# Kernel optimization log

Hardware: AMD Instinct MI355X
Metric: run time of the kernel (lower is better)

The kernel has to match this reference:

```python
import jax, jax.numpy as jnp
import numpy as np

N, E, H, T = 50000, 100000, 512, 6  # nodes, edges, hidden_size, num_edge_types


def setup_inputs() -> dict:
    key = jax.random.key(0)
    ks = jax.random.split(key, 14)
    xav = 1.0 / np.sqrt(H)
    return {
        "statement_embeddings": jax.random.normal(ks[0], (N, H), jnp.float32),
        "source_indices": jax.random.randint(ks[1], (E,), 0, N, dtype=jnp.int32),
        "dest_indices": jax.random.randint(ks[2], (E,), 0, N, dtype=jnp.int32),
        "edge_types": jax.random.randint(ks[3], (E,), 0, T, dtype=jnp.int32),
        "num_nodes": N,
        "hidden_size": H,
        # edge_dense: Dense(features=6*H), xavier_uniform kernel, tiny-normal bias
        "W_edge": jax.random.uniform(ks[4], (H, T * H), jnp.float32, -1.0, 1.0) * np.sqrt(6.0 / (H + T * H)),
        "b_edge": jax.random.normal(ks[5], (T * H,), jnp.float32) * 1e-6,
        # GRUCell params (flax convention: input denses have bias; hidden r/z denses no bias; hidden n dense has bias)
        "W_ir": jax.random.normal(ks[6], (H, H), jnp.float32) * xav,
        "W_iz": jax.random.normal(ks[7], (H, H), jnp.float32) * xav,
        "W_in": jax.random.normal(ks[8], (H, H), jnp.float32) * xav,
        "b_ir": jnp.zeros((H,), jnp.float32),
        "b_iz": jnp.zeros((H,), jnp.float32),
        "b_in": jnp.zeros((H,), jnp.float32),
        "W_hr": jax.random.normal(ks[9], (H, H), jnp.float32) * xav,
        "W_hz": jax.random.normal(ks[10], (H, H), jnp.float32) * xav,
        "W_hn": jax.random.normal(ks[11], (H, H), jnp.float32) * xav,
        "b_hn": jnp.zeros((H,), jnp.float32),
    }


def reference(statement_embeddings, source_indices, dest_indices, edge_types,
              num_nodes, hidden_size,
              W_edge, b_edge,
              W_ir, W_iz, W_in, b_ir, b_iz, b_in,
              W_hr, W_hz, W_hn, b_hn):
    num_edge_types = 6
    # gather source node embeddings: [E, H]
    src = statement_embeddings[source_indices]
    # per-edge dense to all edge types: [E, T*H] -> [E, T, H]
    all_types = (src @ W_edge + b_edge).reshape(-1, num_edge_types, hidden_size)
    # select the slice for each edge's type: [E, H]
    msgs = jnp.take_along_axis(all_types, edge_types[:, None, None], axis=1)[:, 0, :]
    # scatter-add to destination nodes: [N, H]
    proposed = jax.ops.segment_sum(msgs, dest_indices, num_segments=num_nodes)
    # GRU update: inputs=proposed, carry=statement_embeddings
    h = statement_embeddings
    r = jax.nn.sigmoid(proposed @ W_ir + b_ir + h @ W_hr)
    z = jax.nn.sigmoid(proposed @ W_iz + b_iz + h @ W_hz)
    n = jnp.tanh(proposed @ W_in + b_in + r * (h @ W_hn + b_hn))
    return (1.0 - z) * n + z * h
```

## Files before the change

### kernel.cpp

```cpp
#include <hip/hip_runtime.h>
#include <hip/hip_bf16.h>
#include <math.h>

#define H 512
#define NT 6

#define EBM 128
#define EBN 128
#define EBK 32
#define GBM 128
#define GBN 64
#define GBK 32

typedef short bf16x8 __attribute__((ext_vector_type(8)));
typedef float f32x4 __attribute__((ext_vector_type(4)));

__device__ __forceinline__ float sigmoidf_(float x) { return 1.0f / (1.0f + expf(-x)); }

__device__ __forceinline__ unsigned short f2bf(float f) {
    unsigned int u = __float_as_uint(f);
    u = (u + 0x7FFF + ((u >> 16) & 1)) >> 16;
    return (unsigned short)u;
}

__device__ __forceinline__ void glds16(const void* g, void* l) {
    __builtin_amdgcn_global_load_lds((const __attribute__((address_space(1))) unsigned int*)g,
                                     (__attribute__((address_space(3))) unsigned int*)l,
                                     16, 0, 0);
}

__global__ void hist_kernel(const int* __restrict__ etype, int E, int* __restrict__ meta) {
    __shared__ int lh[NT];
    if (threadIdx.x < NT) lh[threadIdx.x] = 0;
    __syncthreads();
    int i = blockIdx.x * blockDim.x + threadIdx.x;
    if (i < E) atomicAdd(&lh[etype[i]], 1);
    __syncthreads();
    if (threadIdx.x < NT) {
        int c = lh[threadIdx.x];
        if (c) atomicAdd(&meta[threadIdx.x], c);
    }
}

__global__ void prefix_kernel(int* __restrict__ meta) {
    if (threadIdx.x == 0 && blockIdx.x == 0) {
        int acc = 0;
        for (int t = 0; t < NT; ++t) {
            meta[8 + t]  = acc;
            meta[16 + t] = acc;
            acc += ((meta[t] + EBM - 1) / EBM) * EBM;
        }
        meta[8 + NT] = acc;
    }
}

__global__ void scatter_perm_kernel(const int* __restrict__ etype, int E,
                                    int* __restrict__ meta, int* __restrict__ perm) {
    __shared__ int lcount[NT];
    __shared__ int lbase[NT];
    const int tid = threadIdx.x;
    if (tid < NT) lcount[tid] = 0;
    __syncthreads();
    int i = blockIdx.x * blockDim.x + tid;
    int t = 0, rank = 0;
    if (i < E) {
        t = etype[i];
        rank = atomicAdd(&lcount[t], 1);
    }
    __syncthreads();
    if (tid < NT) {
        int c = lcount[tid];
        lbase[tid] = c ? atomicAdd(&meta[16 + tid], c) : 0;
    }
    __syncthreads();
    if (i < E) perm[lbase[t] + rank] = i;
}

__global__ void conv_bf16_kernel(const float* __restrict__ in, unsigned short* __restrict__ out, int n4) {
    int i = blockIdx.x * blockDim.x + threadIdx.x;
    if (i < n4) {
        float4 v = ((const float4*)in)[i];
        ushort4 o;
        o.x = f2bf(v.x); o.y = f2bf(v.y); o.z = f2bf(v.z); o.w = f2bf(v.w);
        ((ushort4*)out)[i] = o;
    }
}

__global__ void conv_gru_w_kernel(const float* __restrict__ Wir, const float* __restrict__ Wiz,
                                  const float* __restrict__ Win, const float* __restrict__ Whr,
                                  const float* __restrict__ Whz, const float* __restrict__ Whn,
                                  unsigned short* __restrict__ Brt, unsigned short* __restrict__ Bzt,
                                  unsigned short* __restrict__ Bnit, unsigned short* __restrict__ Bnht) {
    int idx = blockIdx.x * blockDim.x + threadIdx.x;
    if (idx >= 512 * 1024) return;
    int n = idx >> 10;
    int k = idx & 1023;
    int kk = k & 511;
    const float* wr = (k < 512) ? Wir : Whr;
    const float* wz = (k < 512) ? Wiz : Whz;
    Brt[idx] = f2bf(wr[kk * H + n]);
    Bzt[idx] = f2bf(wz[kk * H + n]);
    if (k < 512) Bnit[n * H + k]  = f2bf(Win[k * H + n]);
    else         Bnht[n * H + kk] = f2bf(Whn[kk * H + n]);
}

__global__ void conv_edge_w_kernel(const float* __restrict__ W_edge, unsigned short* __restrict__ WeT) {
    int idx = blockIdx.x * blockDim.x + threadIdx.x;
    if (idx >= 3072 * 512) return;
    int n = idx >> 9;
    int k = idx & 511;
    WeT[idx] = f2bf(W_edge[(size_t)k * (NT * H) + n]);
}

__global__ __launch_bounds__(256)
void edge_msg_mfma(const unsigned short* __restrict__ emb_bf,
                   const int* __restrict__ src_idx,
                   const int* __restrict__ dst_idx,
                   const float* __restrict__ b_edge,
                   const unsigned short* __restrict__ WeT,
                   const int* __restrict__ meta,
                   const int* __restrict__ perm,
                   float* __restrict__ proposed)
{
    __shared__ short As[2][EBM * EBK];
    __shared__ short Bs[2][EBN * EBK];
    __shared__ int ls_src[EBM];
    __shared__ int ls_dst[EBM];

    const int rowBase = blockIdx.y * EBM;
    if (rowBase >= meta[8 + NT]) return;
    int t = 0;
    while (rowBase >= meta[8 + t + 1]) ++t;

    const int colBase = blockIdx.x * EBN;
    const int tid = threadIdx.x;

    if (tid < EBM) {
        int e = perm[rowBase + tid];
        int s = 0, d = -1;
        if (e >= 0) { s = src_idx[e] * H; d = dst_idx[e] * H; }
        ls_src[tid] = s;
        ls_dst[tid] = d;
    }
    __syncthreads();

    const int lane = tid & 63;
    const int wave = tid >> 6;
    const int wm = (wave >> 1) * 64;
    const int wn = (wave & 1) * 64;
    const int q = lane >> 4;
    const int r = lane & 15;

    const int rA   = tid >> 2;
    const int slot = (tid & 3) * 8;

    const int s0 = ls_src[rA];
    const int s1 = ls_src[64 + rA];
    const size_t b0 = ((size_t)(t * H + colBase + rA)) * H + slot;
    const size_t b1 = ((size_t)(t * H + colBase + 64 + rA)) * H + slot;

    f32x4 acc[4][4];
    #pragma unroll
    for (int i = 0; i < 4; ++i)
        #pragma unroll
        for (int j = 0; j < 4; ++j) acc[i][j] = (f32x4){0.f, 0.f, 0.f, 0.f};

#define ESTAGE(K0, B)                                                   \
    {                                                                   \
        glds16(emb_bf + (size_t)s0 + (K0) + slot, &As[B][tid * 8]);     \
        glds16(emb_bf + (size_t)s1 + (K0) + slot, &As[B][(256 + tid) * 8]); \
        glds16(WeT + b0 + (K0), &Bs[B][tid * 8]);                       \
        glds16(WeT + b1 + (K0), &Bs[B][(256 + tid) * 8]);               \
    }

    ESTAGE(0, 0);
    __syncthreads();
    int cur = 0;

    for (int k0 = 0; k0 < H; k0 += EBK) {
        if (k0 + EBK < H) ESTAGE(k0 + EBK, cur ^ 1);

        bf16x8 a[4];
        #pragma unroll
        for (int i = 0; i < 4; ++i)
            a[i] = *(const bf16x8*)&As[cur][(wm + i * 16 + r) * EBK + q * 8];
        #pragma unroll
        for (int j = 0; j < 4; ++j) {
            bf16x8 b = *(const bf16x8*)&Bs[cur][(wn + j * 16 + r) * EBK + q * 8];
            #pragma unroll
            for (int i = 0; i < 4; ++i)
                acc[i][j] = __builtin_amdgcn_mfma_f32_16x16x32_bf16(a[i], b, acc[i][j], 0, 0, 0);
        }
        __syncthreads();
        cur ^= 1;
    }
#undef ESTAGE

    int cols[4];
    float bias[4];
    #pragma unroll
    for (int j = 0; j < 4; ++j) {
        cols[j] = colBase + wn + j * 16 + r;
        bias[j] = b_edge[t * H + cols[j]];
    }
    #pragma unroll
    for (int i = 0; i < 4; ++i) {
        #pragma unroll
        for (int reg = 0; reg < 4; ++reg) {
            int row = wm + i * 16 + q * 4 + reg;
            int d = ls_dst[row];
            if (d < 0) continue;
            #pragma unroll
            for (int j = 0; j < 4; ++j)
                atomicAdd(&proposed[(size_t)d + cols[j]], acc[i][j][reg] + bias[j]);
        }
    }
}

__global__ __launch_bounds__(256)
void gru_mfma(const unsigned short* __restrict__ prop_bf,
              const unsigned short* __restrict__ emb_bf,
              const float* __restrict__ emb_f32,
              const unsigned short* __restrict__ Brt,
              const unsigned short* __restrict__ Bzt,
              const unsigned short* __restrict__ Bnit,
              const unsigned short* __restrict__ Bnht,
              const float* __restrict__ bir, const float* __restrict__ biz,
              const float* __restrict__ bin, const float* __restrict__ bhn,
              float* __restrict__ out, int N)
{
    __shared__ short As[2][GBM * GBK];
    __shared__ short Brs[2][GBN * GBK];
    __shared__ short Bzs[2][GBN * GBK];
    __shared__ short Bns[2][GBN * GBK];

    int wg = blockIdx.y * gridDim.x + blockIdx.x;
    const int nwg = gridDim.x * gridDim.y;
    if ((nwg & 7) == 0) {
        const int cpx = nwg >> 3;
        wg = (wg & 7) * cpx + (wg >> 3);
    }
    const int rowBase = (wg / gridDim.x) * GBM;
    const int colBase = (wg % gridDim.x) * GBN;

    const int tid = threadIdx.x;
    const int lane = tid & 63;
    const int wave = tid >> 6;
    const int wm = (wave >> 1) * 64;
    const int wn = (wave & 1) * 32;
    const int q = lane >> 4;
    const int r = lane & 15;

    const int rA   = tid >> 2;
    const int slot = (tid & 3) * 8;

    const size_t aOff0  = (size_t)(rowBase + rA) * H + slot;
    const size_t aOff1  = (size_t)(rowBase + 64 + rA) * H + slot;
    const size_t bOffRZ = (size_t)(colBase + rA) * 1024 + slot;
    const size_t bOffN  = (size_t)(colBase + rA) * 512 + slot;

    f32x4 accR[4][2], accZ[4][2], accNI[4][2], accNH[4][2];
    #pragma unroll
    for (int i = 0; i < 4; ++i)
        #pragma unroll
        for (int j = 0; j < 2; ++j) {
            accR[i][j] = (f32x4){0.f, 0.f, 0.f, 0.f};
            accZ[i][j] = accR[i][j];
            accNI[i][j] = accR[i][j];
            accNH[i][j] = accR[i][j];
        }

#define GSTAGE(S, B)                                                     \
    {                                                                    \
        const unsigned short* Asrc_ = ((S) < 16) ? prop_bf : emb_bf;     \
        const unsigned short* Bn_   = ((S) < 16) ? Bnit : Bnht;          \
        const int kk_ = ((S) & 15) * GBK;                                \
        const int k0_ = (S) * GBK;                                       \
        glds16(Asrc_ + aOff0 + kk_, &As[B][tid * 8]);                    \
        glds16(Asrc_ + aOff1 + kk_, &As[B][(256 + tid) * 8]);            \
        glds16(Brt + bOffRZ + k0_, &Brs[B][tid * 8]);                    \
        glds16(Bzt + bOffRZ + k0_, &Bzs[B][tid * 8]);                    \
        glds16(Bn_ + bOffN + kk_, &Bns[B][tid * 8]);                     \
    }

#define GCOMPUTE(ACCN, B)                                                                            \
    {                                                                                                \
        bf16x8 a[4];                                                                                 \
        _Pragma("unroll")                                                                            \
        for (int i = 0; i < 4; ++i)                                                                  \
            a[i] = *(const bf16x8*)&As[B][(wm + i * 16 + r) * GBK + q * 8];                          \
        _Pragma("unroll")                                                                            \
        for (int j = 0; j < 2; ++j) {                                                                \
            bf16x8 br = *(const bf16x8*)&Brs[B][(wn + j * 16 + r) * GBK + q * 8];                    \
            bf16x8 bz = *(const bf16x8*)&Bzs[B][(wn + j * 16 + r) * GBK + q * 8];                    \
            bf16x8 bn = *(const bf16x8*)&Bns[B][(wn + j * 16 + r) * GBK + q * 8];                    \
            _Pragma("unroll")                                                                        \
            for (int i = 0; i < 4; ++i) {                                                            \
                accR[i][j] = __builtin_amdgcn_mfma_f32_16x16x32_bf16(a[i], br, accR[i][j], 0, 0, 0); \
                accZ[i][j] = __builtin_amdgcn_mfma_f32_16x16x32_bf16(a[i], bz, accZ[i][j], 0, 0, 0); \
                ACCN[i][j] = __builtin_amdgcn_mfma_f32_16x16x32_bf16(a[i], bn, ACCN[i][j], 0, 0, 0); \
            }                                                                                        \
        }                                                                                            \
    }

    GSTAGE(0, 0);
    __syncthreads();
    int cur = 0;

    for (int s = 0; s < 16; ++s) {
        GSTAGE(s + 1, cur ^ 1);
        GCOMPUTE(accNI, cur);
        __syncthreads();
        cur ^= 1;
    }
    for (int s = 16; s < 32; ++s) {
        if (s < 31) GSTAGE(s + 1, cur ^ 1);
        GCOMPUTE(accNH, cur);
        __syncthreads();
        cur ^= 1;
    }
#undef GSTAGE
#undef GCOMPUTE

    #pragma unroll
    for (int j = 0; j < 2; ++j) {
        const int col = colBase + wn + j * 16 + r;
        const float vbir = bir[col], vbiz = biz[col], vbin = bin[col], vbhn = bhn[col];
        #pragma unroll
        for (int i = 0; i < 4; ++i) {
            #pragma unroll
            for (int reg = 0; reg < 4; ++reg) {
                const int row = rowBase + wm + i * 16 + q * 4 + reg;
                if (row >= N) continue;
                float rg = sigmoidf_(accR[i][j][reg] + vbir);
                float zg = sigmoidf_(accZ[i][j][reg] + vbiz);
                float ng = tanhf(accNI[i][j][reg] + vbin + rg * (accNH[i][j][reg] + vbhn));
                float h = emb_f32[(size_t)row * H + col];
                out[(size_t)row * H + col] = (1.0f - zg) * ng + zg * h;
            }
        }
    }
}

extern "C" void kernel_launch(void* const* d_in, const int* in_sizes, int n_in,
                              void* d_out, int out_size, void* d_ws, size_t ws_size,
                              hipStream_t stream) {
    const float* emb     = (const float*)d_in[0];
    const int*   src_idx = (const int*)d_in[1];
    const int*   dst_idx = (const int*)d_in[2];
    const int*   etype   = (const int*)d_in[3];
    const float* W_edge  = (const float*)d_in[6];
    const float* b_edge  = (const float*)d_in[7];
    const float* Wir = (const float*)d_in[8];
    const float* Wiz = (const float*)d_in[9];
    const float* Win = (const float*)d_in[10];
    const float* bir = (const float*)d_in[11];
    const float* biz = (const float*)d_in[12];
    const float* bin = (const float*)d_in[13];
    const float* Whr = (const float*)d_in[14];
    const float* Whz = (const float*)d_in[15];
    const float* Whn = (const float*)d_in[16];
    const float* bhn = (const float*)d_in[17];

    const int E = in_sizes[1];
    const int N = in_sizes[0] / H;
    const int NH = N * H;

    char* ws = (char*)d_ws;
    float*          proposed = (float*)ws;                       ws += (size_t)NH * 4;
    unsigned short* prop_bf  = (unsigned short*)ws;              ws += (size_t)NH * 2;
    unsigned short* emb_bf   = (unsigned short*)ws;              ws += (size_t)NH * 2;
    unsigned short* Brt      = (unsigned short*)ws;              ws += 512 * 1024 * 2;
    unsigned short* Bzt      = (unsigned short*)ws;              ws += 512 * 1024 * 2;
    unsigned short* Bnit     = (unsigned short*)ws;              ws += 512 * 512 * 2;
    unsigned short* Bnht     = (unsigned short*)ws;              ws += 512 * 512 * 2;
    unsigned short* WeT      = (unsigned short*)ws;              ws += 3072 * 512 * 2;
    int*            meta     = (int*)ws;                         ws += 32 * 4;
    int*            perm     = (int*)ws;
    const int maxRowTiles = (E + EBM - 1) / EBM + NT;

    hipMemsetAsync(proposed, 0, (size_t)NH * 4, stream);
    hipMemsetAsync(meta, 0, 32 * 4, stream);
    hipMemsetAsync(perm, 0xFF, (size_t)maxRowTiles * EBM * 4, stream);

    const int n4 = NH / 4;
    conv_bf16_kernel<<<(n4 + 255) / 256, 256, 0, stream>>>(emb, emb_bf, n4);
    conv_gru_w_kernel<<<(512 * 1024 + 255) / 256, 256, 0, stream>>>(
        Wir, Wiz, Win, Whr, Whz, Whn, Brt, Bzt, Bnit, Bnht);
    conv_edge_w_kernel<<<(3072 * 512 + 255) / 256, 256, 0, stream>>>(W_edge, WeT);

    hist_kernel<<<(E + 255) / 256, 256, 0, stream>>>(etype, E, meta);
    prefix_kernel<<<1, 64, 0, stream>>>(meta);
    scatter_perm_kernel<<<(E + 255) / 256, 256, 0, stream>>>(etype, E, meta, perm);

    dim3 egrid(H / EBN, maxRowTiles);
    edge_msg_mfma<<<egrid, 256, 0, stream>>>(emb_bf, src_idx, dst_idx, b_edge, WeT,
                                             meta, perm, proposed);

    conv_bf16_kernel<<<(n4 + 255) / 256, 256, 0, stream>>>(proposed, prop_bf, n4);

    dim3 ggrid(H / GBN, (N + GBM - 1) / GBM);
    gru_mfma<<<ggrid, 256, 0, stream>>>(prop_bf, emb_bf, emb, Brt, Bzt, Bnit, Bnht,
                                        bir, biz, bin, bhn, (float*)d_out, N);
}
```

Before: 877.7 us.

## Deepen LDS pipelining to four buffers with vmcnt-based waits and single barrier

Both the edge-message GEMM and the GRU GEMM move from double-buffered LDS staging to a four-slot ring that prefetches two stages ahead. Each iteration now waits only until the current stage's async global-to-LDS loads have landed (s_waitcnt vmcnt with an outstanding-load count) and uses one barrier, instead of a full __syncthreads at the end of every step. The aim is to keep more loads in flight and hide global memory latency behind MFMA work. In exchange LDS use doubles, which may lower occupancy. Correctness depends on the hard-coded vmcnt values matching the number of loads issued per stage, and on the four-slot ring leaving enough distance that a slot is not overwritten while a slower wave is still reading it.

```diff
diff --git a/kernel.cpp b/kernel.cpp
--- a/kernel.cpp
+++ b/kernel.cpp
@@ -28,6 +28,13 @@
                                      (__attribute__((address_space(3))) unsigned int*)l,
                                      16, 0, 0);
 }
+
+#define WAITBAR(N)                                         \
+    {                                                      \
+        asm volatile("s_waitcnt vmcnt(" #N ")" ::: "memory"); \
+        __builtin_amdgcn_s_barrier();                      \
+        asm volatile("" ::: "memory");                     \
+    }
 
 __global__ void hist_kernel(const int* __restrict__ etype, int E, int* __restrict__ meta) {
     __shared__ int lh[NT];
@@ -122,8 +129,8 @@
                    const int* __restrict__ perm,
                    float* __restrict__ proposed)
 {
-    __shared__ short As[2][EBM * EBK];
-    __shared__ short Bs[2][EBN * EBK];
+    __shared__ short As[4][EBM * EBK];
+    __shared__ short Bs[4][EBN * EBK];
     __shared__ int ls_src[EBM];
     __shared__ int ls_dst[EBM];
 
@@ -165,36 +172,43 @@
         #pragma unroll
         for (int j = 0; j < 4; ++j) acc[i][j] = (f32x4){0.f, 0.f, 0.f, 0.f};
 
-#define ESTAGE(K0, B)                                                   \
-    {                                                                   \
-        glds16(emb_bf + (size_t)s0 + (K0) + slot, &As[B][tid * 8]);     \
-        glds16(emb_bf + (size_t)s1 + (K0) + slot, &As[B][(256 + tid) * 8]); \
-        glds16(WeT + b0 + (K0), &Bs[B][tid * 8]);                       \
-        glds16(WeT + b1 + (K0), &Bs[B][(256 + tid) * 8]);               \
+#define ESTAGE(S, B)                                                        \
+    {                                                                       \
+        const int k0_ = (S) * EBK;                                          \
+        glds16(emb_bf + (size_t)s0 + k0_ + slot, &As[B][tid * 8]);          \
+        glds16(emb_bf + (size_t)s1 + k0_ + slot, &As[B][(256 + tid) * 8]);  \
+        glds16(WeT + b0 + k0_, &Bs[B][tid * 8]);                            \
+        glds16(WeT + b1 + k0_, &Bs[B][(256 + tid) * 8]);                    \
+    }
+
+#define ECOMPUTE(B)                                                                          \
+    {                                                                                        \
+        bf16x8 a[4];                                                                         \
+        _Pragma("unroll")                                                                    \
+        for (int i = 0; i < 4; ++i)                                                          \
+            a[i] = *(const bf16x8*)&As[B][(wm + i * 16 + r) * EBK + q * 8];                  \
+        _Pragma("unroll")                                                                    \
+        for (int j = 0; j < 4; ++j) {                                                        \
+            bf16x8 b = *(const bf16x8*)&Bs[B][(wn + j * 16 + r) * EBK + q * 8];              \
+            _Pragma("unroll")                                                                \
+            for (int i = 0; i < 4; ++i)                                                      \
+                acc[i][j] = __builtin_amdgcn_mfma_f32_16x16x32_bf16(a[i], b, acc[i][j], 0, 0, 0); \
+        }                                                                                    \
     }
 
     ESTAGE(0, 0);
-    __syncthreads();
-    int cur = 0;
-
-    for (int k0 = 0; k0 < H; k0 += EBK) {
-        if (k0 + EBK < H) ESTAGE(k0 + EBK, cur ^ 1);
-
-        bf16x8 a[4];
-        #pragma unroll
-        for (int i = 0; i < 4; ++i)
-            a[i] = *(const bf16x8*)&As[cur][(wm + i * 16 + r) * EBK + q * 8];
-        #pragma unroll
-        for (int j = 0; j < 4; ++j) {
-            bf16x8 b = *(const bf16x8*)&Bs[cur][(wn + j * 16 + r) * EBK + q * 8];
-            #pragma unroll
-            for (int i = 0; i < 4; ++i)
-                acc[i][j] = __builtin_amdgcn_mfma_f32_16x16x32_bf16(a[i], b, acc[i][j], 0, 0, 0);
-        }
-        __syncthreads();
-        cur ^= 1;
-    }
+    ESTAGE(1, 1);
+    for (int s = 0; s < 14; ++s) {
+        ESTAGE(s + 2, (s + 2) & 3);
+        WAITBAR(8);
+        ECOMPUTE(s & 3);
+    }
+    WAITBAR(4);
+    ECOMPUTE(2);
+    WAITBAR(0);
+    ECOMPUTE(3);
 #undef ESTAGE
+#undef ECOMPUTE
 
     int cols[4];
     float bias[4];
@@ -229,10 +243,10 @@
               const float* __restrict__ bin, const float* __restrict__ bhn,
               float* __restrict__ out, int N)
 {
-    __shared__ short As[2][GBM * GBK];
-    __shared__ short Brs[2][GBN * GBK];
-    __shared__ short Bzs[2][GBN * GBK];
-    __shared__ short Bns[2][GBN * GBK];
+    __shared__ short As[4][GBM * GBK];
+    __shared__ short Brs[4][GBN * GBK];
+    __shared__ short Bzs[4][GBN * GBK];
+    __shared__ short Bns[4][GBN * GBK];
 
     int wg = blockIdx.y * gridDim.x + blockIdx.x;
     const int nwg = gridDim.x * gridDim.y;
@@ -304,21 +318,21 @@
     }
 
     GSTAGE(0, 0);
-    __syncthreads();
-    int cur = 0;
-
+    GSTAGE(1, 1);
     for (int s = 0; s < 16; ++s) {
-        GSTAGE(s + 1, cur ^ 1);
-        GCOMPUTE(accNI, cur);
-        __syncthreads();
-        cur ^= 1;
-    }
-    for (int s = 16; s < 32; ++s) {
-        if (s < 31) GSTAGE(s + 1, cur ^ 1);
-        GCOMPUTE(accNH, cur);
-        __syncthreads();
-        cur ^= 1;
-    }
+        GSTAGE(s + 2, (s + 2) & 3);
+        WAITBAR(10);
+        GCOMPUTE(accNI, s & 3);
+    }
+    for (int s = 16; s < 30; ++s) {
+        GSTAGE(s + 2, (s + 2) & 3);
+        WAITBAR(10);
+        GCOMPUTE(accNH, s & 3);
+    }
+    WAITBAR(5);
+    GCOMPUTE(accNH, 2);
+    WAITBAR(0);
+    GCOMPUTE(accNH, 3);
 #undef GSTAGE
 #undef GCOMPUTE
 
```

After: 994.8 us. 1.13x slower.

## Triple-buffer GEMM pipelines, interleave activations, use fixed-point int atomics

Applied to the files above, without the earlier changes.

Both MFMA GEMMs move from a double-buffered loop with a full barrier each step to a fully unrolled three-stage LDS pipeline. Each step waits with s_waitcnt vmcnt(N) plus a raw barrier, so global-to-LDS loads stay in flight during compute. Proposed and embedding activations are stored interleaved in one row-concatenated bf16 buffer [prop|emb] with a unified transposed N-gate weight, which simplifies GRU staging. The scatter-add now uses integer atomics on values scaled by 65536, trading float atomics for fixed-point rounding and possible overflow on large sums. The GRU kernel also gains a launch-bounds occupancy hint of 2.

```diff
diff --git a/kernel.cpp b/kernel.cpp
--- a/kernel.cpp
+++ b/kernel.cpp
@@ -12,6 +12,9 @@
 #define GBN 64
 #define GBK 32
 
+#define PSCALE 65536.0f
+#define PINV   (1.0f / 65536.0f)
+
 typedef short bf16x8 __attribute__((ext_vector_type(8)));
 typedef float f32x4 __attribute__((ext_vector_type(4)));
 
@@ -28,6 +31,13 @@
                                      (__attribute__((address_space(3))) unsigned int*)l,
                                      16, 0, 0);
 }
+
+#define WAITBAR(N)                                                        \
+    {                                                                     \
+        asm volatile("s_waitcnt vmcnt(" #N ") lgkmcnt(0)" ::: "memory");  \
+        __builtin_amdgcn_s_barrier();                                     \
+        asm volatile("" ::: "memory");                                    \
+    }
 
 __global__ void hist_kernel(const int* __restrict__ etype, int E, int* __restrict__ meta) {
     __shared__ int lh[NT];
@@ -76,13 +86,29 @@
     if (i < E) perm[lbase[t] + rank] = i;
 }
 
-__global__ void conv_bf16_kernel(const float* __restrict__ in, unsigned short* __restrict__ out, int n4) {
+__global__ void conv_to_ah(const float* __restrict__ in, unsigned short* __restrict__ AH,
+                           int n4, int half) {
     int i = blockIdx.x * blockDim.x + threadIdx.x;
     if (i < n4) {
         float4 v = ((const float4*)in)[i];
         ushort4 o;
         o.x = f2bf(v.x); o.y = f2bf(v.y); o.z = f2bf(v.z); o.w = f2bf(v.w);
-        ((ushort4*)out)[i] = o;
+        int row = i >> 7;
+        int c4  = i & 127;
+        ((ushort4*)AH)[row * 256 + half * 128 + c4] = o;
+    }
+}
+
+__global__ void conv_i2ah(const int* __restrict__ in, unsigned short* __restrict__ AH, int n4) {
+    int i = blockIdx.x * blockDim.x + threadIdx.x;
+    if (i < n4) {
+        int4 v = ((const int4*)in)[i];
+        ushort4 o;
+        o.x = f2bf((float)v.x * PINV); o.y = f2bf((float)v.y * PINV);
+        o.z = f2bf((float)v.z * PINV); o.w = f2bf((float)v.w * PINV);
+        int row = i >> 7;
+        int c4  = i & 127;
+        ((ushort4*)AH)[row * 256 + c4] = o;
     }
 }
 
@@ -90,7 +116,7 @@
                                   const float* __restrict__ Win, const float* __restrict__ Whr,
                                   const float* __restrict__ Whz, const float* __restrict__ Whn,
                                   unsigned short* __restrict__ Brt, unsigned short* __restrict__ Bzt,
-                                  unsigned short* __restrict__ Bnit, unsigned short* __restrict__ Bnht) {
+                                  unsigned short* __restrict__ Bnt) {
     int idx = blockIdx.x * blockDim.x + threadIdx.x;
     if (idx >= 512 * 1024) return;
     int n = idx >> 10;
@@ -98,10 +124,10 @@
     int kk = k & 511;
     const float* wr = (k < 512) ? Wir : Whr;
     const float* wz = (k < 512) ? Wiz : Whz;
+    const float* wn = (k < 512) ? Win : Whn;
     Brt[idx] = f2bf(wr[kk * H + n]);
     Bzt[idx] = f2bf(wz[kk * H + n]);
-    if (k < 512) Bnit[n * H + k]  = f2bf(Win[k * H + n]);
-    else         Bnht[n * H + kk] = f2bf(Whn[kk * H + n]);
+    Bnt[idx] = f2bf(wn[kk * H + n]);
 }
 
 __global__ void conv_edge_w_kernel(const float* __restrict__ W_edge, unsigned short* __restrict__ WeT) {
@@ -113,17 +139,17 @@
 }
 
 __global__ __launch_bounds__(256)
-void edge_msg_mfma(const unsigned short* __restrict__ emb_bf,
+void edge_msg_mfma(const unsigned short* __restrict__ AH,
                    const int* __restrict__ src_idx,
                    const int* __restrict__ dst_idx,
                    const float* __restrict__ b_edge,
                    const unsigned short* __restrict__ WeT,
                    const int* __restrict__ meta,
                    const int* __restrict__ perm,
-                   float* __restrict__ proposed)
+                   int* __restrict__ proposed)
 {
-    __shared__ short As[2][EBM * EBK];
-    __shared__ short Bs[2][EBN * EBK];
+    __shared__ short As[3][EBM * EBK];
+    __shared__ short Bs[3][EBN * EBK];
     __shared__ int ls_src[EBM];
     __shared__ int ls_dst[EBM];
 
@@ -137,8 +163,8 @@
 
     if (tid < EBM) {
         int e = perm[rowBase + tid];
-        int s = 0, d = -1;
-        if (e >= 0) { s = src_idx[e] * H; d = dst_idx[e] * H; }
+        int s = 512, d = -1;
+        if (e >= 0) { s = src_idx[e] * 1024 + 512; d = dst_idx[e] * H; }
         ls_src[tid] = s;
         ls_dst[tid] = d;
     }
@@ -165,36 +191,45 @@
         #pragma unroll
         for (int j = 0; j < 4; ++j) acc[i][j] = (f32x4){0.f, 0.f, 0.f, 0.f};
 
-#define ESTAGE(K0, B)                                                   \
-    {                                                                   \
-        glds16(emb_bf + (size_t)s0 + (K0) + slot, &As[B][tid * 8]);     \
-        glds16(emb_bf + (size_t)s1 + (K0) + slot, &As[B][(256 + tid) * 8]); \
-        glds16(WeT + b0 + (K0), &Bs[B][tid * 8]);                       \
-        glds16(WeT + b1 + (K0), &Bs[B][(256 + tid) * 8]);               \
+#define ESTAGE(S, B)                                                         \
+    {                                                                        \
+        glds16(AH + (size_t)s0 + (S) * EBK + slot, &As[B][tid * 8]);         \
+        glds16(AH + (size_t)s1 + (S) * EBK + slot, &As[B][(256 + tid) * 8]); \
+        glds16(WeT + b0 + (S) * EBK, &Bs[B][tid * 8]);                       \
+        glds16(WeT + b1 + (S) * EBK, &Bs[B][(256 + tid) * 8]);               \
+    }
+
+#define ECOMPUTE(B)                                                                               \
+    {                                                                                             \
+        bf16x8 a[4];                                                                              \
+        _Pragma("unroll")                                                                         \
+        for (int i = 0; i < 4; ++i)                                                               \
+            a[i] = *(const bf16x8*)&As[B][(wm + i * 16 + r) * EBK + q * 8];                       \
+        _Pragma("unroll")                                                                         \
+        for (int j = 0; j < 4; ++j) {                                                             \
+            bf16x8 b = *(const bf16x8*)&Bs[B][(wn + j * 16 + r) * EBK + q * 8];                   \
+            _Pragma("unroll")                                                                     \
+            for (int i = 0; i < 4; ++i)                                                           \
+                acc[i][j] = __builtin_amdgcn_mfma_f32_16x16x32_bf16(a[i], b, acc[i][j], 0, 0, 0); \
+        }                                                                                         \
+    }
+
+#define ESTEP(S)                         \
+    {                                    \
+        WAITBAR(4);                      \
+        ESTAGE((S) + 2, ((S) + 2) % 3);  \
+        ECOMPUTE((S) % 3);               \
     }
 
     ESTAGE(0, 0);
-    __syncthreads();
-    int cur = 0;
-
-    for (int k0 = 0; k0 < H; k0 += EBK) {
-        if (k0 + EBK < H) ESTAGE(k0 + EBK, cur ^ 1);
-
-        bf16x8 a[4];
-        #pragma unroll
-        for (int i = 0; i < 4; ++i)
-            a[i] = *(const bf16x8*)&As[cur][(wm + i * 16 + r) * EBK + q * 8];
-        #pragma unroll
-        for (int j = 0; j < 4; ++j) {
-            bf16x8 b = *(const bf16x8*)&Bs[cur][(wn + j * 16 + r) * EBK + q * 8];
-            #pragma unroll
-            for (int i = 0; i < 4; ++i)
-                acc[i][j] = __builtin_amdgcn_mfma_f32_16x16x32_bf16(a[i], b, acc[i][j], 0, 0, 0);
-        }
-        __syncthreads();
-        cur ^= 1;
-    }
+    ESTAGE(1, 1);
+    ESTEP(0)  ESTEP(1)  ESTEP(2)  ESTEP(3)  ESTEP(4)  ESTEP(5)  ESTEP(6)
+    ESTEP(7)  ESTEP(8)  ESTEP(9)  ESTEP(10) ESTEP(11) ESTEP(12) ESTEP(13)
+    { WAITBAR(4); ECOMPUTE(2); }
+    { WAITBAR(0); ECOMPUTE(0); }
 #undef ESTAGE
+#undef ECOMPUTE
+#undef ESTEP
 
     int cols[4];
     float bias[4];
@@ -212,27 +247,26 @@
             if (d < 0) continue;
             #pragma unroll
             for (int j = 0; j < 4; ++j)
-                atomicAdd(&proposed[(size_t)d + cols[j]], acc[i][j][reg] + bias[j]);
+                atomicAdd(&proposed[(size_t)d + cols[j]],
+                          __float2int_rn((acc[i][j][reg] + bias[j]) * PSCALE));
         }
     }
 }
 
-__global__ __launch_bounds__(256)
-void gru_mfma(const unsigned short* __restrict__ prop_bf,
-              const unsigned short* __restrict__ emb_bf,
+__global__ __launch_bounds__(256, 2)
+void gru_mfma(const unsigned short* __restrict__ AH,
               const float* __restrict__ emb_f32,
               const unsigned short* __restrict__ Brt,
               const unsigned short* __restrict__ Bzt,
-              const unsigned short* __restrict__ Bnit,
-              const unsigned short* __restrict__ Bnht,
+              const unsigned short* __restrict__ Bnt,
               const float* __restrict__ bir, const float* __restrict__ biz,
               const float* __restrict__ bin, const float* __restrict__ bhn,
               float* __restrict__ out, int N)
 {
-    __shared__ short As[2][GBM * GBK];
-    __shared__ short Brs[2][GBN * GBK];
-    __shared__ short Bzs[2][GBN * GBK];
-    __shared__ short Bns[2][GBN * GBK];
+    __shared__ short As[3][GBM * GBK];
+    __shared__ short Brs[3][GBN * GBK];
+    __shared__ short Bzs[3][GBN * GBK];
+    __shared__ short Bns[3][GBN * GBK];
 
     int wg = blockIdx.y * gridDim.x + blockIdx.x;
     const int nwg = gridDim.x * gridDim.y;
@@ -254,10 +288,9 @@
     const int rA   = tid >> 2;
     const int slot = (tid & 3) * 8;
 
-    const size_t aOff0  = (size_t)(rowBase + rA) * H + slot;
-    const size_t aOff1  = (size_t)(rowBase + 64 + rA) * H + slot;
-    const size_t bOffRZ = (size_t)(colBase + rA) * 1024 + slot;
-    const size_t bOffN  = (size_t)(colBase + rA) * 512 + slot;
+    const size_t aOff0 = (size_t)(rowBase + rA) * 1024 + slot;
+    const size_t aOff1 = (size_t)(rowBase + 64 + rA) * 1024 + slot;
+    const size_t bOff  = (size_t)(colBase + rA) * 1024 + slot;
 
     f32x4 accR[4][2], accZ[4][2], accNI[4][2], accNH[4][2];
     #pragma unroll
@@ -270,17 +303,13 @@
             accNH[i][j] = accR[i][j];
         }
 
-#define GSTAGE(S, B)                                                     \
-    {                                                                    \
-        const unsigned short* Asrc_ = ((S) < 16) ? prop_bf : emb_bf;     \
-        const unsigned short* Bn_   = ((S) < 16) ? Bnit : Bnht;          \
-        const int kk_ = ((S) & 15) * GBK;                                \
-        const int k0_ = (S) * GBK;                                       \
-        glds16(Asrc_ + aOff0 + kk_, &As[B][tid * 8]);                    \
-        glds16(Asrc_ + aOff1 + kk_, &As[B][(256 + tid) * 8]);            \
-        glds16(Brt + bOffRZ + k0_, &Brs[B][tid * 8]);                    \
-        glds16(Bzt + bOffRZ + k0_, &Bzs[B][tid * 8]);                    \
-        glds16(Bn_ + bOffN + kk_, &Bns[B][tid * 8]);                     \
+#define GSTAGE(S, B)                                             \
+    {                                                            \
+        glds16(AH + aOff0 + (S) * GBK, &As[B][tid * 8]);         \
+        glds16(AH + aOff1 + (S) * GBK, &As[B][(256 + tid) * 8]); \
+        glds16(Brt + bOff + (S) * GBK, &Brs[B][tid * 8]);        \
+        glds16(Bzt + bOff + (S) * GBK, &Bzs[B][tid * 8]);        \
+        glds16(Bnt + bOff + (S) * GBK, &Bns[B][tid * 8]);        \
     }
 
 #define GCOMPUTE(ACCN, B)                                                                            \
@@ -303,24 +332,28 @@
         }                                                                                            \
     }
 
+#define GSTEP(S, ACCN)                   \
+    {                                    \
+        WAITBAR(5);                      \
+        GSTAGE((S) + 2, ((S) + 2) % 3);  \
+        GCOMPUTE(ACCN, (S) % 3);         \
+    }
+
     GSTAGE(0, 0);
-    __syncthreads();
-    int cur = 0;
-
-    for (int s = 0; s < 16; ++s) {
-        GSTAGE(s + 1, cur ^ 1);
-        GCOMPUTE(accNI, cur);
-        __syncthreads();
-        cur ^= 1;
-    }
-    for (int s = 16; s < 32; ++s) {
-        if (s < 31) GSTAGE(s + 1, cur ^ 1);
-        GCOMPUTE(accNH, cur);
-        __syncthreads();
-        cur ^= 1;
-    }
+    GSTAGE(1, 1);
+    GSTEP(0,  accNI) GSTEP(1,  accNI) GSTEP(2,  accNI) GSTEP(3,  accNI)
+    GSTEP(4,  accNI) GSTEP(5,  accNI) GSTEP(6,  accNI) GSTEP(7,  accNI)
+    GSTEP(8,  accNI) GSTEP(9,  accNI) GSTEP(10, accNI) GSTEP(11, accNI)
+    GSTEP(12, accNI) GSTEP(13, accNI) GSTEP(14, accNI) GSTEP(15, accNI)
+    GSTEP(16, accNH) GSTEP(17, accNH) GSTEP(18, accNH) GSTEP(19, accNH)
+    GSTEP(20, accNH) GSTEP(21, accNH) GSTEP(22, accNH) GSTEP(23, accNH)
+    GSTEP(24, accNH) GSTEP(25, accNH) GSTEP(26, accNH) GSTEP(27, accNH)
+    GSTEP(28, accNH) GSTEP(29, accNH)
+    { WAITBAR(5); GCOMPUTE(accNH, 0); }
+    { WAITBAR(0); GCOMPUTE(accNH, 1); }
 #undef GSTAGE
 #undef GCOMPUTE
+#undef GSTEP
 
     #pragma unroll
     for (int j = 0; j < 2; ++j) {
@@ -367,13 +400,11 @@
     const int NH = N * H;
 
     char* ws = (char*)d_ws;
-    float*          proposed = (float*)ws;                       ws += (size_t)NH * 4;
-    unsigned short* prop_bf  = (unsigned short*)ws;              ws += (size_t)NH * 2;
-    unsigned short* emb_bf   = (unsigned short*)ws;              ws += (size_t)NH * 2;
+    int*            proposed = (int*)ws;                         ws += (size_t)NH * 4;
+    unsigned short* AH       = (unsigned short*)ws;              ws += (size_t)NH * 2 * 2;
     unsigned short* Brt      = (unsigned short*)ws;              ws += 512 * 1024 * 2;
     unsigned short* Bzt      = (unsigned short*)ws;              ws += 512 * 1024 * 2;
-    unsigned short* Bnit     = (unsigned short*)ws;              ws += 512 * 512 * 2;
-    unsigned short* Bnht     = (unsigned short*)ws;              ws += 512 * 512 * 2;
+    unsigned short* Bnt      = (unsigned short*)ws;              ws += 512 * 1024 * 2;
     unsigned short* WeT      = (unsigned short*)ws;              ws += 3072 * 512 * 2;
     int*            meta     = (int*)ws;                         ws += 32 * 4;
     int*            perm     = (int*)ws;
@@ -384,9 +415,9 @@
     hipMemsetAsync(perm, 0xFF, (size_t)maxRowTiles * EBM * 4, stream);
 
     const int n4 = NH / 4;
-    conv_bf16_kernel<<<(n4 + 255) / 256, 256, 0, stream>>>(emb, emb_bf, n4);
+    conv_to_ah<<<(n4 + 255) / 256, 256, 0, stream>>>(emb, AH, n4, 1);
     conv_gru_w_kernel<<<(512 * 1024 + 255) / 256, 256, 0, stream>>>(
-        Wir, Wiz, Win, Whr, Whz, Whn, Brt, Bzt, Bnit, Bnht);
+        Wir, Wiz, Win, Whr, Whz, Whn, Brt, Bzt, Bnt);
     conv_edge_w_kernel<<<(3072 * 512 + 255) / 256, 256, 0, stream>>>(W_edge, WeT);
 
     hist_kernel<<<(E + 255) / 256, 256, 0, stream>>>(etype, E, meta);
@@ -394,12 +425,12 @@
     scatter_perm_kernel<<<(E + 255) / 256, 256, 0, stream>>>(etype, E, meta, perm);
 
     dim3 egrid(H / EBN, maxRowTiles);
-    edge_msg_mfma<<<egrid, 256, 0, stream>>>(emb_bf, src_idx, dst_idx, b_edge, WeT,
+    edge_msg_mfma<<<egrid, 256, 0, stream>>>(AH, src_idx, dst_idx, b_edge, WeT,
                                              meta, perm, proposed);
 
-    conv_bf16_kernel<<<(n4 + 255) / 256, 256, 0, stream>>>(proposed, prop_bf, n4);
+    conv_i2ah<<<(n4 + 255) / 256, 256, 0, stream>>>(proposed, AH, n4);
 
     dim3 ggrid(H / GBN, (N + GBM - 1) / GBM);
-    gru_mfma<<<ggrid, 256, 0, stream>>>(prop_bf, emb_bf, emb, Brt, Bzt, Bnit, Bnht,
+    gru_mfma<<<ggrid, 256, 0, stream>>>(AH, emb, Brt, Bzt, Bnt,
                                         bir, biz, bin, bhn, (float*)d_out, N);
 }
```

Measured after the change: 781.6 us. -10.9%, faster.
